# Performance work log

Hardware: AMD Instinct MI355X
Metric: run time of the kernel (lower is better)

The kernel has to match this reference:

```python
import jax, jax.numpy as jnp
import numpy as np

B, T, KD, QD, AD, VD, W = 16, 4096, 1024, 1024, 512, 1024, 8


def moving_sum(x, back, forward):
    # x: [B, T] -> windowed sum over [t-back, t+forward], matches F.conv1d with ones filter
    xp = jnp.pad(x, ((0, 0), (back, forward)))[:, None, :]
    filt = jnp.ones((1, 1, back + forward + 1), x.dtype)
    y = jax.lax.conv_general_dilated(xp, filt, (1,), 'VALID')
    return y[:, 0, :]


def setup_inputs() -> dict:
    key = jax.random.key(0)
    ks = jax.random.split(key, 16)
    inp = {
        'key': jax.random.normal(ks[0], (B, T, KD), jnp.float32),
        'value': jax.random.normal(ks[1], (B, T, VD), jnp.float32),
        'query': jax.random.normal(ks[2], (B, 1, QD), jnp.float32),
        'noise': jax.random.normal(ks[3], (B, T), jnp.float32),
        'Wk_mono': jax.random.normal(ks[4], (KD, AD), jnp.float32) * (KD ** -0.5),
        'b_mono': jnp.zeros((AD,), jnp.float32),
        'Wq_mono': jax.random.normal(ks[5], (QD, AD), jnp.float32) * (QD ** -0.5),
        'Wk_chunk': jax.random.normal(ks[6], (KD, AD), jnp.float32) * (KD ** -0.5),
        'b_chunk': jnp.zeros((AD,), jnp.float32),
        'Wq_chunk': jax.random.normal(ks[7], (QD, AD), jnp.float32) * (QD ** -0.5),
        'r_mono': jnp.array([-4.0], jnp.float32),
        'r_chunk': jnp.array([-4.0], jnp.float32),
    }
    # weight-normalized v vectors: g = sqrt(1/attn_dim), w = g * v/||v||
    g = (1.0 / AD) ** 0.5
    vm = jax.random.normal(ks[8], (AD,), jnp.float32)
    vc = jax.random.normal(ks[9], (AD,), jnp.float32)
    inp['v_mono'] = g * vm / jnp.linalg.norm(vm)
    inp['v_chunk'] = g * vc / jnp.linalg.norm(vc)
    return inp


def _forward(key, value, query, noise, Wk_mono, b_mono, Wq_mono, v_mono, r_mono,
             Wk_chunk, b_chunk, Wq_chunk, v_chunk, r_chunk):
    bs, kmax = key.shape[0], key.shape[1]
    # aw_prev default: one-hot at position 0
    aw_prev = jnp.zeros((bs, kmax), key.dtype).at[:, 0].set(1.0)

    # monotonic energy: [B, T]
    qm = jnp.einsum('bqd,da->bqa', query, Wq_mono)  # [B,1,A], broadcasts over T
    e_mono = jnp.einsum('bta,a->bt', jnp.tanh(key @ Wk_mono + b_mono + qm), v_mono) + r_mono

    # parallel mode: sigmoid with additive gaussian noise
    p_choose = jax.nn.sigmoid(e_mono + noise)
    # safe_cumprod with the original's exclusive_cumsum (prepends ONES, drops last)
    log1mp = jnp.log(jnp.clip(1.0 - p_choose, 1e-10, 1.0))
    shifted = jnp.concatenate([jnp.ones((bs, 1), key.dtype), log1mp[:, :-1]], axis=1)
    cumprod_1mp = jnp.exp(jnp.cumsum(shifted, axis=1))
    aw = p_choose * cumprod_1mp * jnp.cumsum(
        aw_prev / jnp.clip(cumprod_1mp, 1e-10, 1.0), axis=1)

    # chunk energy
    qc = jnp.einsum('bqd,da->bqa', query, Wq_chunk)
    e_chunk = jnp.einsum('bta,a->bt', jnp.tanh(key @ Wk_chunk + b_chunk + qc), v_chunk) + r_chunk

    # efficient chunkwise attention
    u = e_chunk - jnp.max(e_chunk, axis=1, keepdims=True)
    softmax_exp = jnp.maximum(jnp.exp(u), 1e-5)
    denom = moving_sum(softmax_exp, back=W - 1, forward=0)
    beta = softmax_exp * moving_sum(aw / denom, back=0, forward=W - 1)

    cv = jnp.einsum('bt,btd->bd', beta, value)[:, None, :]  # [B,1,VD]
    return cv, aw[..., None]


def reference(key, value, query, noise, Wk_mono, b_mono, Wq_mono, v_mono, r_mono,
              Wk_chunk, b_chunk, Wq_chunk, v_chunk, r_chunk):
    return _forward(key, value, query, noise, Wk_mono, b_mono, Wq_mono, v_mono, r_mono,
                    Wk_chunk, b_chunk, Wq_chunk, v_chunk, r_chunk)
```

## Files before the change

kernel.cpp:

```cpp
#include <hip/hip_runtime.h>
#include <hip/hip_bf16.h>
#include <math.h>

#define B_   16
#define T_   4096
#define KD_  1024
#define AD_  512
#define VD_  1024

typedef float f32x4 __attribute__((ext_vector_type(4)));
typedef short s16x8 __attribute__((ext_vector_type(8)));

static __device__ __forceinline__ short f2bf(float f) {
    __hip_bfloat16 h = __float2bfloat16(f);
    return __builtin_bit_cast(short, h);
}

static __device__ __forceinline__ float fast_tanh(float x) {
    x = fminf(fmaxf(x, -15.f), 15.f);
    float e = __expf(2.f * x);
    return (e - 1.f) / (e + 1.f);
}

static __device__ __forceinline__ void gload16(const void* g, void* l) {
    __builtin_amdgcn_global_load_lds(
        (const __attribute__((address_space(1))) void*)(g),
        (__attribute__((address_space(3))) void*)(l), 16, 0, 0);
}


__global__ __launch_bounds__(256) void cvt_key_blk_kernel(
    const float* __restrict__ key, short* __restrict__ keyB) {
    const size_t nchunk = (size_t)B_ * T_ * KD_ / 8;
    size_t stride = (size_t)gridDim.x * 256;
    for (size_t g = (size_t)blockIdx.x * 256 + threadIdx.x; g < nchunk; g += stride) {
        const float* p = key + g * 8;
        f32x4 f0 = *reinterpret_cast<const f32x4*>(p);
        f32x4 f1 = *reinterpret_cast<const f32x4*>(p + 4);
        s16x8 h;
        h[0] = f2bf(f0[0]); h[1] = f2bf(f0[1]); h[2] = f2bf(f0[2]); h[3] = f2bf(f0[3]);
        h[4] = f2bf(f1[0]); h[5] = f2bf(f1[1]); h[6] = f2bf(f1[2]); h[7] = f2bf(f1[3]);
        size_t m = g >> 7;
        int kc = (int)(g & 127);
        size_t mt = m >> 8;
        int r = (int)(m & 255);
        int kt = kc >> 2;
        int sub = kc & 3;
        int c = (r << 2) | (sub ^ ((r >> 1) & 3));
        *reinterpret_cast<s16x8*>(keyB + (((mt * 32 + kt) * 1024 + c) << 3)) = h;
    }
}

__global__ __launch_bounds__(256) void qproj_kernel(
    const float* __restrict__ query,
    const float* __restrict__ Wq_mono, const float* __restrict__ b_mono,
    const float* __restrict__ Wq_chunk, const float* __restrict__ b_chunk,
    float* __restrict__ qb) {
    __shared__ float red[4][64];
    int b = blockIdx.x;
    int mat = blockIdx.y;
    int ac = blockIdx.z;
    const float* Wq = mat ? Wq_chunk : Wq_mono;
    const float* bb = mat ? b_chunk : b_mono;
    int al = threadIdx.x & 63;
    int dg = threadIdx.x >> 6;
    int a = ac * 64 + al;
    const float* q = query + b * KD_ + dg * 256;
    const float* wp = Wq + (size_t)(dg * 256) * AD_ + a;
    float s = 0.f;
#pragma unroll 4
    for (int d = 0; d < 256; ++d)
        s += q[d] * wp[(size_t)d * AD_];
    red[dg][al] = s;
    __syncthreads();
    if (dg == 0) {
        float t = red[0][al] + red[1][al] + red[2][al] + red[3][al];
        qb[(mat * B_ + b) * AD_ + a] = t + bb[a];
    }
}

__global__ __launch_bounds__(256) void wtrans_kernel(
    const float* __restrict__ Wk_mono, const float* __restrict__ Wk_chunk,
    short* __restrict__ WkTB) {
    __shared__ float tile[32][33];
    int n0 = blockIdx.x * 32;
    int k0 = blockIdx.y * 32;
    int tx = threadIdx.x;
    int ty = threadIdx.y;
    int tid = ty * 32 + tx;
    const float* src;
    int nloc;
    if (n0 < 512) { src = Wk_mono;  nloc = n0; }
    else          { src = Wk_chunk; nloc = n0 - 512; }
#pragma unroll
    for (int i = 0; i < 4; ++i) {
        int k = ty + i * 8;
        tile[k][tx] = src[(size_t)(k0 + k) * AD_ + nloc + tx];
    }
    __syncthreads();
    if (tid < 128) {
        int r = tid >> 2;
        int sub = tid & 3;
        s16x8 h;
#pragma unroll
        for (int j = 0; j < 8; ++j)
            h[j] = f2bf(tile[sub * 8 + j][r]);
        int n = n0 + r;
        int nblk = n >> 8;
        int rloc = n & 255;
        int kt = k0 >> 5;
        int c = (rloc << 2) | (sub ^ ((rloc >> 1) & 3));
        *reinterpret_cast<s16x8*>(WkTB + (((size_t)(nblk * 32 + kt) * 1024 + c) << 3)) = h;
    }
}

__global__ __launch_bounds__(1024, 4) void gemm_e_kernel(
    const short* __restrict__ keyB,
    const short* __restrict__ WkTB,
    const float* __restrict__ qb,
    const float* __restrict__ v_mono, const float* __restrict__ v_chunk,
    float* __restrict__ e_ws ) {
    __shared__ short As[2][1024 * 8];
    __shared__ short Bs[2][1024 * 8];
    int tid = threadIdx.x;
    int bid = blockIdx.x;
    int swz = (bid & 7) * 128 + (bid >> 3);
    int mt = swz >> 2;
    int nt = swz & 3;
    int mBase = mt * 256;
    int nBase = nt * 256;
    int lane = tid & 63;
    int wid = tid >> 6;
    int wr = wid >> 2, wc = wid & 3;
    int col16 = lane & 15, g4 = lane >> 4;

    const short* pA = keyB + ((size_t)mt * 32 * 1024 + tid) * 8;
    const short* pB = WkTB + ((size_t)nt * 32 * 1024 + tid) * 8;
    int sAB = (wid * 64) * 8;

    int aoff[4], boff[4];
#pragma unroll
    for (int m = 0; m < 4; ++m) {
        int row = wr * 64 + m * 16 + col16;
        aoff[m] = (row * 4 + (g4 ^ ((row >> 1) & 3))) * 8;
    }
#pragma unroll
    for (int n = 0; n < 4; ++n) {
        int row = wc * 64 + n * 16 + col16;
        boff[n] = (row * 4 + (g4 ^ ((row >> 1) & 3))) * 8;
    }

    f32x4 zero4 = {0.f, 0.f, 0.f, 0.f};
    f32x4 acc[4][4];
#pragma unroll
    for (int m = 0; m < 4; ++m)
#pragma unroll
        for (int n = 0; n < 4; ++n) acc[m][n] = zero4;

    gload16(pA, &As[0][sAB]);
    gload16(pB, &Bs[0][sAB]);
    pA += 8192; pB += 8192;
    __syncthreads();

    int cur = 0;
    for (int kt = 0; kt < 31; ++kt) {
        int nxt = cur ^ 1;
        gload16(pA, &As[nxt][sAB]);
        gload16(pB, &Bs[nxt][sAB]);
        pA += 8192; pB += 8192;
        s16x8 af[4], bfr[4];
#pragma unroll
        for (int m = 0; m < 4; ++m)
            af[m] = *reinterpret_cast<const s16x8*>(&As[cur][aoff[m]]);
#pragma unroll
        for (int n = 0; n < 4; ++n)
            bfr[n] = *reinterpret_cast<const s16x8*>(&Bs[cur][boff[n]]);
#pragma unroll
        for (int m = 0; m < 4; ++m)
#pragma unroll
            for (int n = 0; n < 4; ++n)
                acc[m][n] = __builtin_amdgcn_mfma_f32_16x16x32_bf16(af[m], bfr[n], acc[m][n], 0, 0, 0);
        __syncthreads();
        cur = nxt;
    }
    {
        s16x8 af[4], bfr[4];
#pragma unroll
        for (int m = 0; m < 4; ++m)
            af[m] = *reinterpret_cast<const s16x8*>(&As[cur][aoff[m]]);
#pragma unroll
        for (int n = 0; n < 4; ++n)
            bfr[n] = *reinterpret_cast<const s16x8*>(&Bs[cur][boff[n]]);
#pragma unroll
        for (int m = 0; m < 4; ++m)
#pragma unroll
            for (int n = 0; n < 4; ++n)
                acc[m][n] = __builtin_amdgcn_mfma_f32_16x16x32_bf16(af[m], bfr[n], acc[m][n], 0, 0, 0);
    }

    int bIdx = mBase >> 12;
    int matrix = nBase >> 9;
    int aBase = (nBase & 511) + wc * 64 + col16;
    const float* qbRow = qb + (matrix * B_ + bIdx) * AD_;
    const float* vv = matrix ? v_chunk : v_mono;
    float* eArr = e_ws + matrix * (B_ * T_);
    float qcol[4], vcol[4];
#pragma unroll
    for (int n = 0; n < 4; ++n) {
        int a = aBase + n * 16;
        qcol[n] = qbRow[a];
        vcol[n] = vv[a];
    }
#pragma unroll
    for (int m = 0; m < 4; ++m) {
        float s0 = 0.f, s1 = 0.f, s2 = 0.f, s3 = 0.f;
#pragma unroll
        for (int n = 0; n < 4; ++n) {
            s0 += fast_tanh(acc[m][n][0] + qcol[n]) * vcol[n];
            s1 += fast_tanh(acc[m][n][1] + qcol[n]) * vcol[n];
            s2 += fast_tanh(acc[m][n][2] + qcol[n]) * vcol[n];
            s3 += fast_tanh(acc[m][n][3] + qcol[n]) * vcol[n];
        }
#pragma unroll
        for (int mask = 1; mask < 16; mask <<= 1) {
            s0 += __shfl_xor(s0, mask, 64);
            s1 += __shfl_xor(s1, mask, 64);
            s2 += __shfl_xor(s2, mask, 64);
            s3 += __shfl_xor(s3, mask, 64);
        }
        if (col16 == 0) {
            int rowB = mBase + wr * 64 + m * 16 + g4 * 4;
            atomicAdd(&eArr[rowB + 0], s0);
            atomicAdd(&eArr[rowB + 1], s1);
            atomicAdd(&eArr[rowB + 2], s2);
            atomicAdd(&eArr[rowB + 3], s3);
        }
    }
}

__global__ __launch_bounds__(256) void scan_kernel(
    const float* __restrict__ e_ws,
    const float* __restrict__ noise,
    const float* __restrict__ r_mono, const float* __restrict__ r_chunk,
    float* __restrict__ aw_out, float* __restrict__ beta_out) {
    __shared__ float s_aw[T_];
    __shared__ float s_sexp[T_];
    __shared__ float s_ad[T_];
    __shared__ float s_w[4];
    int b = blockIdx.x;
    int tid = threadIdx.x;
    int lane = tid & 63;
    int wid4 = tid >> 6;
    int t0 = tid * 16;
    const float* em = e_ws + b * T_;
    const float* ec = e_ws + B_ * T_ + b * T_;
    const float* nz = noise + b * T_;
    float rm = r_mono[0], rc = r_chunk[0];

    float pv[16], lp[16];
    float run = 0.f;
#pragma unroll
    for (int j = 0; j < 16; ++j) {
        float x = em[t0 + j] + rm + nz[t0 + j];
        float p = 1.f / (1.f + expf(-x));
        pv[j] = p;
        float om = fminf(fmaxf(1.f - p, 1e-10f), 1.f);
        lp[j] = run;
        run += logf(om);
    }
    float x = run;
#pragma unroll
    for (int off = 1; off < 64; off <<= 1) {
        float y = __shfl_up(x, off, 64);
        if (lane >= off) x += y;
    }
    if (lane == 63) s_w[wid4] = x;
    __syncthreads();
    float wbase = 0.f;
#pragma unroll
    for (int i = 0; i < 3; ++i) if (i < wid4) wbase += s_w[i];
    float base = 1.f + (wbase + x - run);
#pragma unroll
    for (int j = 0; j < 16; ++j) {
        float aw = pv[j] * expf(base + lp[j]);
        s_aw[t0 + j] = aw;
        aw_out[b * T_ + t0 + j] = aw;
    }
    float evs[16];
    float lmax = -INFINITY;
#pragma unroll
    for (int j = 0; j < 16; ++j) {
        float v = ec[t0 + j] + rc;
        evs[j] = v;
        lmax = fmaxf(lmax, v);
    }
#pragma unroll
    for (int off = 1; off < 64; off <<= 1)
        lmax = fmaxf(lmax, __shfl_xor(lmax, off, 64));
    __syncthreads();
    if (lane == 0) s_w[wid4] = lmax;
    __syncthreads();
    float mx = fmaxf(fmaxf(s_w[0], s_w[1]), fmaxf(s_w[2], s_w[3]));
#pragma unroll
    for (int j = 0; j < 16; ++j)
        s_sexp[t0 + j] = fmaxf(expf(evs[j] - mx), 1e-5f);
    __syncthreads();
#pragma unroll
    for (int j = 0; j < 16; ++j) {
        int t = t0 + j;
        int lo = t - 7; if (lo < 0) lo = 0;
        float d = 0.f;
        for (int i = lo; i <= t; ++i) d += s_sexp[i];
        s_ad[t] = s_aw[t] / d;
    }
    __syncthreads();
#pragma unroll
    for (int j = 0; j < 16; ++j) {
        int t = t0 + j;
        int hi = t + 7; if (hi > T_ - 1) hi = T_ - 1;
        float m2 = 0.f;
        for (int i = t; i <= hi; ++i) m2 += s_ad[i];
        beta_out[b * T_ + t] = s_sexp[t] * m2;
    }
}

__global__ __launch_bounds__(256) void cv_kernel(
    const float* __restrict__ value,
    const float* __restrict__ beta,
    float* __restrict__ cv) {
    __shared__ float s_beta[128];
    int b = blockIdx.x;
    int tc = blockIdx.y;
    int tid = threadIdx.x;
    int t0 = tc * 128;
    if (tid < 128) s_beta[tid] = beta[b * T_ + t0 + tid];
    __syncthreads();
    int d0 = tid * 4;
    f32x4 acc = {0.f, 0.f, 0.f, 0.f};
    const float* vp = value + (size_t)(b * T_ + t0) * VD_ + d0;
#pragma unroll 4
    for (int i = 0; i < 128; ++i) {
        f32x4 v = *reinterpret_cast<const f32x4*>(vp + (size_t)i * VD_);
        float bt = s_beta[i];
        acc[0] += bt * v[0];
        acc[1] += bt * v[1];
        acc[2] += bt * v[2];
        acc[3] += bt * v[3];
    }
    atomicAdd(&cv[b * VD_ + d0 + 0], acc[0]);
    atomicAdd(&cv[b * VD_ + d0 + 1], acc[1]);
    atomicAdd(&cv[b * VD_ + d0 + 2], acc[2]);
    atomicAdd(&cv[b * VD_ + d0 + 3], acc[3]);
}

extern "C" void kernel_launch(void* const* d_in, const int* in_sizes, int n_in,
                              void* d_out, int out_size, void* d_ws, size_t ws_size,
                              hipStream_t stream) {
    const float* key      = (const float*)d_in[0];
    const float* value    = (const float*)d_in[1];
    const float* query    = (const float*)d_in[2];
    const float* noise    = (const float*)d_in[3];
    const float* Wk_mono  = (const float*)d_in[4];
    const float* b_mono   = (const float*)d_in[5];
    const float* Wq_mono  = (const float*)d_in[6];
    const float* Wk_chunk = (const float*)d_in[7];
    const float* b_chunk  = (const float*)d_in[8];
    const float* Wq_chunk = (const float*)d_in[9];
    const float* r_mono   = (const float*)d_in[10];
    const float* r_chunk  = (const float*)d_in[11];
    const float* v_mono   = (const float*)d_in[12];
    const float* v_chunk  = (const float*)d_in[13];
    float* out = (float*)d_out;

    char* ws = (char*)d_ws;
    size_t off = 0;
    float* e_ws = (float*)(ws + off); off += 2 * B_ * T_ * sizeof(float);
    float* qb   = (float*)(ws + off); off += 2 * B_ * AD_ * sizeof(float);
    short* WkTB = (short*)(ws + off); off += (size_t)KD_ * KD_ * 2;
    float* beta = (float*)(ws + off); off += B_ * T_ * sizeof(float);
    short* keyB = (short*)(ws + off);

    hipMemsetAsync(e_ws, 0, 2 * B_ * T_ * sizeof(float), stream);
    hipMemsetAsync(out, 0, B_ * VD_ * sizeof(float), stream);

    qproj_kernel<<<dim3(16, 2, 8), 256, 0, stream>>>(query, Wq_mono, b_mono, Wq_chunk, b_chunk, qb);
    wtrans_kernel<<<dim3(32, 32), dim3(32, 8), 0, stream>>>(Wk_mono, Wk_chunk, WkTB);
    cvt_key_blk_kernel<<<4096, 256, 0, stream>>>(key, keyB);
    gemm_e_kernel<<<1024, 1024, 0, stream>>>(keyB, WkTB, qb, v_mono, v_chunk, e_ws);
    scan_kernel<<<16, 256, 0, stream>>>(e_ws, noise, r_mono, r_chunk, out + B_ * VD_, beta);
    cv_kernel<<<dim3(16, 32), 256, 0, stream>>>(value, beta, out);
}
```

Baseline: 376.9 us.

## Restructure bf16 GEMM into 8-wave ping-pong pipeline with 64-wide K tiles

The key and weight pre-layouts change from 32-wide to 64-wide K tiles with an 8-way XOR swizzle. The energy GEMM moves from 16 waves with 64x64 warp tiles to 8 waves with 128x64 warp tiles. Its main loop becomes a hand-scheduled pipeline: interleaved half-tile global-to-LDS loads, explicit vmcnt waits, sched barriers and raised priority around MFMA clusters. This aims to hide load latency and cut LDS reads and barriers per MFMA. The cost is higher register pressure from 32 accumulators per thread and fragile manual scheduling.

```diff
diff --git a/kernel.cpp b/kernel.cpp
--- a/kernel.cpp
+++ b/kernel.cpp
@@ -44,10 +44,10 @@
         int kc = (int)(g & 127);
         size_t mt = m >> 8;
         int r = (int)(m & 255);
-        int kt = kc >> 2;
-        int sub = kc & 3;
-        int c = (r << 2) | (sub ^ ((r >> 1) & 3));
-        *reinterpret_cast<s16x8*>(keyB + (((mt * 32 + kt) * 1024 + c) << 3)) = h;
+        int ktile = kc >> 3;
+        int sub = kc & 7;
+        int c = (r << 3) | (sub ^ (r & 7));
+        *reinterpret_cast<s16x8*>(keyB + (((mt * 16 + ktile) * 2048 + c) << 3)) = h;
     }
 }
 
@@ -99,29 +99,76 @@
     }
     __syncthreads();
     if (tid < 128) {
-        int r = tid >> 2;
-        int sub = tid & 3;
+        int rl = tid >> 2;
+        int sub2 = tid & 3;
         s16x8 h;
 #pragma unroll
         for (int j = 0; j < 8; ++j)
-            h[j] = f2bf(tile[sub * 8 + j][r]);
-        int n = n0 + r;
-        int nblk = n >> 8;
+            h[j] = f2bf(tile[sub2 * 8 + j][rl]);
+        int n = n0 + rl;
+        int nt = n >> 8;
         int rloc = n & 255;
-        int kt = k0 >> 5;
-        int c = (rloc << 2) | (sub ^ ((rloc >> 1) & 3));
-        *reinterpret_cast<s16x8*>(WkTB + (((size_t)(nblk * 32 + kt) * 1024 + c) << 3)) = h;
-    }
-}
-
-__global__ __launch_bounds__(1024, 4) void gemm_e_kernel(
+        int ktile = k0 >> 6;
+        int sub = ((k0 & 63) >> 3) + sub2;
+        int c = (rloc << 3) | (sub ^ (rloc & 7));
+        *reinterpret_cast<s16x8*>(WkTB + (((size_t)(nt * 16 + ktile) * 2048 + c) << 3)) = h;
+    }
+}
+
+#define SBAR __builtin_amdgcn_sched_barrier(0)
+#define BAR  do { SBAR; __builtin_amdgcn_s_barrier(); SBAR; } while (0)
+#define VM6  asm volatile("s_waitcnt vmcnt(6)" ::: "memory")
+
+#define STAGE_A(buf, kt, h) do { \
+    const short* _g = aT + (((size_t)(kt) * 2048 + (h) * 1024) << 3); \
+    gload16(_g + tid * 8,        &As[buf][(((h) * 1024 + wid * 64)) * 8]); \
+    gload16(_g + (512 + tid) * 8, &As[buf][(((h) * 1024 + 512 + wid * 64)) * 8]); \
+} while (0)
+
+#define STAGE_B(buf, kt, h) do { \
+    const short* _g = bT + (((size_t)(kt) * 2048 + (h) * 1024) << 3); \
+    gload16(_g + tid * 8,        &Bs[buf][(((h) * 1024 + wid * 64)) * 8]); \
+    gload16(_g + (512 + tid) * 8, &Bs[buf][(((h) * 1024 + 512 + wid * 64)) * 8]); \
+} while (0)
+
+#define DS_A(bb, mh) do { \
+    _Pragma("unroll") \
+    for (int _j = 0; _j < 4; ++_j) { \
+        aR[_j][0] = *reinterpret_cast<const s16x8*>(&As[bb][aoff[(mh) * 4 + _j]]); \
+        aR[_j][1] = *reinterpret_cast<const s16x8*>(&As[bb][aoff[(mh) * 4 + _j] ^ 32]); \
+    } \
+} while (0)
+
+#define DS_B(bb, nh) do { \
+    _Pragma("unroll") \
+    for (int _j = 0; _j < 2; ++_j) { \
+        bR[_j][0] = *reinterpret_cast<const s16x8*>(&Bs[bb][boff[(nh) * 2 + _j]]); \
+        bR[_j][1] = *reinterpret_cast<const s16x8*>(&Bs[bb][boff[(nh) * 2 + _j] ^ 32]); \
+    } \
+} while (0)
+
+#define MMA(mh, nh) do { \
+    __builtin_amdgcn_s_setprio(1); \
+    _Pragma("unroll") \
+    for (int _j = 0; _j < 4; ++_j) \
+    _Pragma("unroll") \
+    for (int _n = 0; _n < 2; ++_n) { \
+        acc[(mh) * 4 + _j][(nh) * 2 + _n] = __builtin_amdgcn_mfma_f32_16x16x32_bf16( \
+            aR[_j][0], bR[_n][0], acc[(mh) * 4 + _j][(nh) * 2 + _n], 0, 0, 0); \
+        acc[(mh) * 4 + _j][(nh) * 2 + _n] = __builtin_amdgcn_mfma_f32_16x16x32_bf16( \
+            aR[_j][1], bR[_n][1], acc[(mh) * 4 + _j][(nh) * 2 + _n], 0, 0, 0); \
+    } \
+    __builtin_amdgcn_s_setprio(0); \
+} while (0)
+
+__global__ __launch_bounds__(512) void gemm_e_kernel(
     const short* __restrict__ keyB,
     const short* __restrict__ WkTB,
     const float* __restrict__ qb,
     const float* __restrict__ v_mono, const float* __restrict__ v_chunk,
     float* __restrict__ e_ws ) {
-    __shared__ short As[2][1024 * 8];
-    __shared__ short Bs[2][1024 * 8];
+    __shared__ short As[2][16384];
+    __shared__ short Bs[2][16384];
     int tid = threadIdx.x;
     int bid = blockIdx.x;
     int swz = (bid & 7) * 128 + (bid >> 3);
@@ -134,69 +181,67 @@
     int wr = wid >> 2, wc = wid & 3;
     int col16 = lane & 15, g4 = lane >> 4;
 
-    const short* pA = keyB + ((size_t)mt * 32 * 1024 + tid) * 8;
-    const short* pB = WkTB + ((size_t)nt * 32 * 1024 + tid) * 8;
-    int sAB = (wid * 64) * 8;
-
-    int aoff[4], boff[4];
-#pragma unroll
-    for (int m = 0; m < 4; ++m) {
-        int row = wr * 64 + m * 16 + col16;
-        aoff[m] = (row * 4 + (g4 ^ ((row >> 1) & 3))) * 8;
-    }
-#pragma unroll
-    for (int n = 0; n < 4; ++n) {
-        int row = wc * 64 + n * 16 + col16;
-        boff[n] = (row * 4 + (g4 ^ ((row >> 1) & 3))) * 8;
-    }
-
-    f32x4 zero4 = {0.f, 0.f, 0.f, 0.f};
-    f32x4 acc[4][4];
-#pragma unroll
-    for (int m = 0; m < 4; ++m)
-#pragma unroll
-        for (int n = 0; n < 4; ++n) acc[m][n] = zero4;
-
-    gload16(pA, &As[0][sAB]);
-    gload16(pB, &Bs[0][sAB]);
-    pA += 8192; pB += 8192;
-    __syncthreads();
-
-    int cur = 0;
-    for (int kt = 0; kt < 31; ++kt) {
-        int nxt = cur ^ 1;
-        gload16(pA, &As[nxt][sAB]);
-        gload16(pB, &Bs[nxt][sAB]);
-        pA += 8192; pB += 8192;
-        s16x8 af[4], bfr[4];
-#pragma unroll
-        for (int m = 0; m < 4; ++m)
-            af[m] = *reinterpret_cast<const s16x8*>(&As[cur][aoff[m]]);
-#pragma unroll
-        for (int n = 0; n < 4; ++n)
-            bfr[n] = *reinterpret_cast<const s16x8*>(&Bs[cur][boff[n]]);
-#pragma unroll
-        for (int m = 0; m < 4; ++m)
-#pragma unroll
-            for (int n = 0; n < 4; ++n)
-                acc[m][n] = __builtin_amdgcn_mfma_f32_16x16x32_bf16(af[m], bfr[n], acc[m][n], 0, 0, 0);
-        __syncthreads();
-        cur = nxt;
-    }
-    {
-        s16x8 af[4], bfr[4];
-#pragma unroll
-        for (int m = 0; m < 4; ++m)
-            af[m] = *reinterpret_cast<const s16x8*>(&As[cur][aoff[m]]);
-#pragma unroll
-        for (int n = 0; n < 4; ++n)
-            bfr[n] = *reinterpret_cast<const s16x8*>(&Bs[cur][boff[n]]);
-#pragma unroll
-        for (int m = 0; m < 4; ++m)
-#pragma unroll
-            for (int n = 0; n < 4; ++n)
-                acc[m][n] = __builtin_amdgcn_mfma_f32_16x16x32_bf16(af[m], bfr[n], acc[m][n], 0, 0, 0);
-    }
+    const short* aT = keyB + ((size_t)mt * 16 * 2048 << 3);
+    const short* bT = WkTB + ((size_t)nt * 16 * 2048 << 3);
+
+    int aoff[8], boff[4];
+#pragma unroll
+    for (int fi = 0; fi < 8; ++fi) {
+        int row = wr * 128 + fi * 16 + col16;
+        aoff[fi] = ((row << 3) | (g4 ^ (row & 7))) * 8;
+    }
+#pragma unroll
+    for (int fj = 0; fj < 4; ++fj) {
+        int col = wc * 64 + fj * 16 + col16;
+        boff[fj] = ((col << 3) | (g4 ^ (col & 7))) * 8;
+    }
+
+    f32x4 acc[8][4];
+#pragma unroll
+    for (int i = 0; i < 8; ++i)
+#pragma unroll
+        for (int j = 0; j < 4; ++j) acc[i][j] = (f32x4){0.f, 0.f, 0.f, 0.f};
+
+    s16x8 aR[4][2], bR[2][2];
+
+    STAGE_A(0, 0, 0); STAGE_B(0, 0, 0); STAGE_B(0, 0, 1); STAGE_A(0, 0, 1);
+    STAGE_A(1, 1, 0); STAGE_B(1, 1, 1); STAGE_A(1, 1, 1);
+    VM6;
+    BAR;
+
+    for (int it = 0; it < 8; ++it) {
+        int t1 = 2 * it + 1;
+        int t2 = 2 * it + 2 > 15 ? 15 : 2 * it + 2;
+        int t3 = 2 * it + 3 > 15 ? 15 : 2 * it + 3;
+        DS_A(0, 0); DS_B(0, 0);
+        STAGE_B(1, t1, 0);
+        BAR; MMA(0, 0); BAR;
+        DS_B(0, 1);
+        STAGE_A(0, t2, 0);
+        BAR; MMA(0, 1); BAR;
+        DS_A(0, 1);
+        STAGE_B(0, t2, 1);
+        BAR; MMA(1, 1); BAR;
+        DS_B(0, 0);
+        STAGE_A(0, t2, 1);
+        VM6;
+        BAR; MMA(1, 0); BAR;
+        DS_A(1, 0); DS_B(1, 0);
+        STAGE_B(0, t2, 0);
+        BAR; MMA(0, 0); BAR;
+        DS_B(1, 1);
+        STAGE_A(1, t3, 0);
+        BAR; MMA(0, 1); BAR;
+        DS_A(1, 1);
+        STAGE_B(1, t3, 1);
+        BAR; MMA(1, 1); BAR;
+        DS_B(1, 0);
+        STAGE_A(1, t3, 1);
+        VM6;
+        BAR; MMA(1, 0); BAR;
+    }
+
+    asm volatile("s_waitcnt vmcnt(0)" ::: "memory");
 
     int bIdx = mBase >> 12;
     int matrix = nBase >> 9;
@@ -212,14 +257,14 @@
         vcol[n] = vv[a];
     }
 #pragma unroll
-    for (int m = 0; m < 4; ++m) {
+    for (int fi = 0; fi < 8; ++fi) {
         float s0 = 0.f, s1 = 0.f, s2 = 0.f, s3 = 0.f;
 #pragma unroll
         for (int n = 0; n < 4; ++n) {
-            s0 += fast_tanh(acc[m][n][0] + qcol[n]) * vcol[n];
-            s1 += fast_tanh(acc[m][n][1] + qcol[n]) * vcol[n];
-            s2 += fast_tanh(acc[m][n][2] + qcol[n]) * vcol[n];
-            s3 += fast_tanh(acc[m][n][3] + qcol[n]) * vcol[n];
+            s0 += fast_tanh(acc[fi][n][0] + qcol[n]) * vcol[n];
+            s1 += fast_tanh(acc[fi][n][1] + qcol[n]) * vcol[n];
+            s2 += fast_tanh(acc[fi][n][2] + qcol[n]) * vcol[n];
+            s3 += fast_tanh(acc[fi][n][3] + qcol[n]) * vcol[n];
         }
 #pragma unroll
         for (int mask = 1; mask < 16; mask <<= 1) {
@@ -229,7 +274,7 @@
             s3 += __shfl_xor(s3, mask, 64);
         }
         if (col16 == 0) {
-            int rowB = mBase + wr * 64 + m * 16 + g4 * 4;
+            int rowB = mBase + wr * 128 + fi * 16 + g4 * 4;
             atomicAdd(&eArr[rowB + 0], s0);
             atomicAdd(&eArr[rowB + 1], s1);
             atomicAdd(&eArr[rowB + 2], s2);
@@ -386,7 +431,7 @@
     qproj_kernel<<<dim3(16, 2, 8), 256, 0, stream>>>(query, Wq_mono, b_mono, Wq_chunk, b_chunk, qb);
     wtrans_kernel<<<dim3(32, 32), dim3(32, 8), 0, stream>>>(Wk_mono, Wk_chunk, WkTB);
     cvt_key_blk_kernel<<<4096, 256, 0, stream>>>(key, keyB);
-    gemm_e_kernel<<<1024, 1024, 0, stream>>>(keyB, WkTB, qb, v_mono, v_chunk, e_ws);
+    gemm_e_kernel<<<1024, 512, 0, stream>>>(keyB, WkTB, qb, v_mono, v_chunk, e_ws);
     scan_kernel<<<16, 256, 0, stream>>>(e_ws, noise, r_mono, r_chunk, out + B_ * VD_, beta);
     cv_kernel<<<dim3(16, 32), 256, 0, stream>>>(value, beta, out);
 }
```

Result: faster. 360.9 us (-4.2%).

## Fuse prep kernels and shrink GEMM block to 4 waves with 128x128 warp tiles

Applied to the files above, without the earlier changes.

The key conversion, weight transpose, query projection and two memsets are merged into one prep kernel launch, which removes several launch and memset overheads. The GEMM block goes from 16 waves at 64x64 each to 4 waves at 128x128 each over the same 256x256 tile. This raises register reuse of the LDS fragments per wave but needs 256 accumulator registers per lane, which risks spilling or lower occupancy. Each thread now issues four LDS-direct loads per operand per k-step.

```diff
diff --git a/kernel.cpp b/kernel.cpp
--- a/kernel.cpp
+++ b/kernel.cpp
@@ -29,92 +29,105 @@
 }
 
 
-__global__ __launch_bounds__(256) void cvt_key_blk_kernel(
-    const float* __restrict__ key, short* __restrict__ keyB) {
-    const size_t nchunk = (size_t)B_ * T_ * KD_ / 8;
-    size_t stride = (size_t)gridDim.x * 256;
-    for (size_t g = (size_t)blockIdx.x * 256 + threadIdx.x; g < nchunk; g += stride) {
-        const float* p = key + g * 8;
-        f32x4 f0 = *reinterpret_cast<const f32x4*>(p);
-        f32x4 f1 = *reinterpret_cast<const f32x4*>(p + 4);
-        s16x8 h;
-        h[0] = f2bf(f0[0]); h[1] = f2bf(f0[1]); h[2] = f2bf(f0[2]); h[3] = f2bf(f0[3]);
-        h[4] = f2bf(f1[0]); h[5] = f2bf(f1[1]); h[6] = f2bf(f1[2]); h[7] = f2bf(f1[3]);
-        size_t m = g >> 7;
-        int kc = (int)(g & 127);
-        size_t mt = m >> 8;
-        int r = (int)(m & 255);
-        int kt = kc >> 2;
-        int sub = kc & 3;
-        int c = (r << 2) | (sub ^ ((r >> 1) & 3));
-        *reinterpret_cast<s16x8*>(keyB + (((mt * 32 + kt) * 1024 + c) << 3)) = h;
-    }
-}
-
-__global__ __launch_bounds__(256) void qproj_kernel(
+__global__ __launch_bounds__(256) void prep_kernel(
+    const float* __restrict__ key, short* __restrict__ keyB,
+    const float* __restrict__ Wk_mono, const float* __restrict__ Wk_chunk,
+    short* __restrict__ WkTB,
     const float* __restrict__ query,
     const float* __restrict__ Wq_mono, const float* __restrict__ b_mono,
     const float* __restrict__ Wq_chunk, const float* __restrict__ b_chunk,
-    float* __restrict__ qb) {
-    __shared__ float red[4][64];
-    int b = blockIdx.x;
-    int mat = blockIdx.y;
-    int ac = blockIdx.z;
-    const float* Wq = mat ? Wq_chunk : Wq_mono;
-    const float* bb = mat ? b_chunk : b_mono;
-    int al = threadIdx.x & 63;
-    int dg = threadIdx.x >> 6;
-    int a = ac * 64 + al;
-    const float* q = query + b * KD_ + dg * 256;
-    const float* wp = Wq + (size_t)(dg * 256) * AD_ + a;
-    float s = 0.f;
+    float* __restrict__ qb,
+    float* __restrict__ e_ws, float* __restrict__ outzero) {
+    int bid = blockIdx.x;
+    int tid = threadIdx.x;
+
+    if (bid < 4096) {
+        const size_t nchunk = (size_t)B_ * T_ * KD_ / 8;
+        size_t stride = (size_t)4096 * 256;
+        for (size_t g = (size_t)bid * 256 + tid; g < nchunk; g += stride) {
+            const float* p = key + g * 8;
+            f32x4 f0 = *reinterpret_cast<const f32x4*>(p);
+            f32x4 f1 = *reinterpret_cast<const f32x4*>(p + 4);
+            s16x8 h;
+            h[0] = f2bf(f0[0]); h[1] = f2bf(f0[1]); h[2] = f2bf(f0[2]); h[3] = f2bf(f0[3]);
+            h[4] = f2bf(f1[0]); h[5] = f2bf(f1[1]); h[6] = f2bf(f1[2]); h[7] = f2bf(f1[3]);
+            size_t m = g >> 7;
+            int kc = (int)(g & 127);
+            size_t mt = m >> 8;
+            int r = (int)(m & 255);
+            int kt = kc >> 2;
+            int sub = kc & 3;
+            int c = (r << 2) | (sub ^ ((r >> 1) & 3));
+            *reinterpret_cast<s16x8*>(keyB + (((mt * 32 + kt) * 1024 + c) << 3)) = h;
+        }
+    } else if (bid < 5120) {
+        __shared__ float tile[32][33];
+        int wbid = bid - 4096;
+        int n0 = (wbid & 31) * 32;
+        int k0 = (wbid >> 5) * 32;
+        int tx = tid & 31;
+        int ty = tid >> 5;
+        const float* src;
+        int nloc;
+        if (n0 < 512) { src = Wk_mono;  nloc = n0; }
+        else          { src = Wk_chunk; nloc = n0 - 512; }
+#pragma unroll
+        for (int i = 0; i < 4; ++i) {
+            int k = ty + i * 8;
+            tile[k][tx] = src[(size_t)(k0 + k) * AD_ + nloc + tx];
+        }
+        __syncthreads();
+        if (tid < 128) {
+            int rl = tid >> 2;
+            int sub = tid & 3;
+            s16x8 h;
+#pragma unroll
+            for (int j = 0; j < 8; ++j)
+                h[j] = f2bf(tile[sub * 8 + j][rl]);
+            int n = n0 + rl;
+            int nt = n >> 8;
+            int rloc = n & 255;
+            int kt = k0 >> 5;
+            int c = (rloc << 2) | (sub ^ ((rloc >> 1) & 3));
+            *reinterpret_cast<s16x8*>(WkTB + (((size_t)(nt * 32 + kt) * 1024 + c) << 3)) = h;
+        }
+    } else if (bid < 5376) {
+        __shared__ float red[4][64];
+        int qbid = bid - 5120;
+        int b = qbid & 15;
+        int mat = (qbid >> 4) & 1;
+        int ac = qbid >> 5;
+        const float* Wq = mat ? Wq_chunk : Wq_mono;
+        const float* bb = mat ? b_chunk : b_mono;
+        int al = tid & 63;
+        int dg = tid >> 6;
+        int a = ac * 64 + al;
+        const float* q = query + b * KD_ + dg * 256;
+        const float* wp = Wq + (size_t)(dg * 256) * AD_ + a;
+        float s = 0.f;
 #pragma unroll 4
-    for (int d = 0; d < 256; ++d)
-        s += q[d] * wp[(size_t)d * AD_];
-    red[dg][al] = s;
-    __syncthreads();
-    if (dg == 0) {
-        float t = red[0][al] + red[1][al] + red[2][al] + red[3][al];
-        qb[(mat * B_ + b) * AD_ + a] = t + bb[a];
-    }
-}
-
-__global__ __launch_bounds__(256) void wtrans_kernel(
-    const float* __restrict__ Wk_mono, const float* __restrict__ Wk_chunk,
-    short* __restrict__ WkTB) {
-    __shared__ float tile[32][33];
-    int n0 = blockIdx.x * 32;
-    int k0 = blockIdx.y * 32;
-    int tx = threadIdx.x;
-    int ty = threadIdx.y;
-    int tid = ty * 32 + tx;
-    const float* src;
-    int nloc;
-    if (n0 < 512) { src = Wk_mono;  nloc = n0; }
-    else          { src = Wk_chunk; nloc = n0 - 512; }
-#pragma unroll
-    for (int i = 0; i < 4; ++i) {
-        int k = ty + i * 8;
-        tile[k][tx] = src[(size_t)(k0 + k) * AD_ + nloc + tx];
-    }
-    __syncthreads();
-    if (tid < 128) {
-        int r = tid >> 2;
-        int sub = tid & 3;
-        s16x8 h;
-#pragma unroll
-        for (int j = 0; j < 8; ++j)
-            h[j] = f2bf(tile[sub * 8 + j][r]);
-        int n = n0 + r;
-        int nblk = n >> 8;
-        int rloc = n & 255;
-        int kt = k0 >> 5;
-        int c = (rloc << 2) | (sub ^ ((rloc >> 1) & 3));
-        *reinterpret_cast<s16x8*>(WkTB + (((size_t)(nblk * 32 + kt) * 1024 + c) << 3)) = h;
-    }
-}
-
-__global__ __launch_bounds__(1024, 4) void gemm_e_kernel(
+        for (int d = 0; d < 256; ++d)
+            s += q[d] * wp[(size_t)d * AD_];
+        red[dg][al] = s;
+        __syncthreads();
+        if (dg == 0) {
+            float t = red[0][al] + red[1][al] + red[2][al] + red[3][al];
+            qb[(mat * B_ + b) * AD_ + a] = t + bb[a];
+        }
+    } else {
+        int zbid = bid - 5376;
+        f32x4 z = {0.f, 0.f, 0.f, 0.f};
+        if (zbid < 128) {
+            float* dst = e_ws + (size_t)zbid * 1024 + tid * 4;
+            *reinterpret_cast<f32x4*>(dst) = z;
+        } else {
+            float* dst = outzero + (size_t)(zbid - 128) * 1024 + tid * 4;
+            *reinterpret_cast<f32x4*>(dst) = z;
+        }
+    }
+}
+
+__global__ __launch_bounds__(256) void gemm_e_kernel(
     const short* __restrict__ keyB,
     const short* __restrict__ WkTB,
     const float* __restrict__ qb,
@@ -131,95 +144,104 @@
     int nBase = nt * 256;
     int lane = tid & 63;
     int wid = tid >> 6;
-    int wr = wid >> 2, wc = wid & 3;
+    int wr = wid >> 1, wc = wid & 1;
     int col16 = lane & 15, g4 = lane >> 4;
 
-    const short* pA = keyB + ((size_t)mt * 32 * 1024 + tid) * 8;
-    const short* pB = WkTB + ((size_t)nt * 32 * 1024 + tid) * 8;
-    int sAB = (wid * 64) * 8;
-
-    int aoff[4], boff[4];
-#pragma unroll
-    for (int m = 0; m < 4; ++m) {
-        int row = wr * 64 + m * 16 + col16;
-        aoff[m] = (row * 4 + (g4 ^ ((row >> 1) & 3))) * 8;
-    }
-#pragma unroll
-    for (int n = 0; n < 4; ++n) {
-        int row = wc * 64 + n * 16 + col16;
-        boff[n] = (row * 4 + (g4 ^ ((row >> 1) & 3))) * 8;
-    }
-
-    f32x4 zero4 = {0.f, 0.f, 0.f, 0.f};
-    f32x4 acc[4][4];
-#pragma unroll
-    for (int m = 0; m < 4; ++m)
-#pragma unroll
-        for (int n = 0; n < 4; ++n) acc[m][n] = zero4;
-
-    gload16(pA, &As[0][sAB]);
-    gload16(pB, &Bs[0][sAB]);
-    pA += 8192; pB += 8192;
+    const short* pA[4];
+    const short* pB[4];
+    int sOff[4];
+#pragma unroll
+    for (int i = 0; i < 4; ++i) {
+        pA[i] = keyB + ((size_t)mt * 32 * 1024 + i * 256 + tid) * 8;
+        pB[i] = WkTB + ((size_t)nt * 32 * 1024 + i * 256 + tid) * 8;
+        sOff[i] = (i * 256 + wid * 64) * 8;
+    }
+
+    int aoff[8], boff[8];
+#pragma unroll
+    for (int fi = 0; fi < 8; ++fi) {
+        int row = wr * 128 + fi * 16 + col16;
+        aoff[fi] = (row * 4 + (g4 ^ ((row >> 1) & 3))) * 8;
+    }
+#pragma unroll
+    for (int fj = 0; fj < 8; ++fj) {
+        int coln = wc * 128 + fj * 16 + col16;
+        boff[fj] = (coln * 4 + (g4 ^ ((coln >> 1) & 3))) * 8;
+    }
+
+    f32x4 acc[8][8];
+#pragma unroll
+    for (int i = 0; i < 8; ++i)
+#pragma unroll
+        for (int j = 0; j < 8; ++j) acc[i][j] = (f32x4){0.f, 0.f, 0.f, 0.f};
+
+#pragma unroll
+    for (int i = 0; i < 4; ++i) {
+        gload16(pA[i], &As[0][sOff[i]]);
+        gload16(pB[i], &Bs[0][sOff[i]]);
+        pA[i] += 8192; pB[i] += 8192;
+    }
     __syncthreads();
 
     int cur = 0;
     for (int kt = 0; kt < 31; ++kt) {
         int nxt = cur ^ 1;
-        gload16(pA, &As[nxt][sAB]);
-        gload16(pB, &Bs[nxt][sAB]);
-        pA += 8192; pB += 8192;
-        s16x8 af[4], bfr[4];
-#pragma unroll
-        for (int m = 0; m < 4; ++m)
-            af[m] = *reinterpret_cast<const s16x8*>(&As[cur][aoff[m]]);
-#pragma unroll
-        for (int n = 0; n < 4; ++n)
-            bfr[n] = *reinterpret_cast<const s16x8*>(&Bs[cur][boff[n]]);
-#pragma unroll
-        for (int m = 0; m < 4; ++m)
-#pragma unroll
-            for (int n = 0; n < 4; ++n)
-                acc[m][n] = __builtin_amdgcn_mfma_f32_16x16x32_bf16(af[m], bfr[n], acc[m][n], 0, 0, 0);
+#pragma unroll
+        for (int i = 0; i < 4; ++i) {
+            gload16(pA[i], &As[nxt][sOff[i]]);
+            gload16(pB[i], &Bs[nxt][sOff[i]]);
+            pA[i] += 8192; pB[i] += 8192;
+        }
+        s16x8 bfr[8];
+#pragma unroll
+        for (int fj = 0; fj < 8; ++fj)
+            bfr[fj] = *reinterpret_cast<const s16x8*>(&Bs[cur][boff[fj]]);
+#pragma unroll
+        for (int fi = 0; fi < 8; ++fi) {
+            s16x8 af = *reinterpret_cast<const s16x8*>(&As[cur][aoff[fi]]);
+#pragma unroll
+            for (int fj = 0; fj < 8; ++fj)
+                acc[fi][fj] = __builtin_amdgcn_mfma_f32_16x16x32_bf16(af, bfr[fj], acc[fi][fj], 0, 0, 0);
+        }
         __syncthreads();
         cur = nxt;
     }
     {
-        s16x8 af[4], bfr[4];
-#pragma unroll
-        for (int m = 0; m < 4; ++m)
-            af[m] = *reinterpret_cast<const s16x8*>(&As[cur][aoff[m]]);
-#pragma unroll
-        for (int n = 0; n < 4; ++n)
-            bfr[n] = *reinterpret_cast<const s16x8*>(&Bs[cur][boff[n]]);
-#pragma unroll
-        for (int m = 0; m < 4; ++m)
-#pragma unroll
-            for (int n = 0; n < 4; ++n)
-                acc[m][n] = __builtin_amdgcn_mfma_f32_16x16x32_bf16(af[m], bfr[n], acc[m][n], 0, 0, 0);
+        s16x8 bfr[8];
+#pragma unroll
+        for (int fj = 0; fj < 8; ++fj)
+            bfr[fj] = *reinterpret_cast<const s16x8*>(&Bs[cur][boff[fj]]);
+#pragma unroll
+        for (int fi = 0; fi < 8; ++fi) {
+            s16x8 af = *reinterpret_cast<const s16x8*>(&As[cur][aoff[fi]]);
+#pragma unroll
+            for (int fj = 0; fj < 8; ++fj)
+                acc[fi][fj] = __builtin_amdgcn_mfma_f32_16x16x32_bf16(af, bfr[fj], acc[fi][fj], 0, 0, 0);
+        }
     }
 
     int bIdx = mBase >> 12;
     int matrix = nBase >> 9;
-    int aBase = (nBase & 511) + wc * 64 + col16;
+    int aBase = (nBase & 511) + wc * 128 + col16;
     const float* qbRow = qb + (matrix * B_ + bIdx) * AD_;
     const float* vv = matrix ? v_chunk : v_mono;
     float* eArr = e_ws + matrix * (B_ * T_);
-    float qcol[4], vcol[4];
-#pragma unroll
-    for (int n = 0; n < 4; ++n) {
-        int a = aBase + n * 16;
-        qcol[n] = qbRow[a];
-        vcol[n] = vv[a];
-    }
-#pragma unroll
-    for (int m = 0; m < 4; ++m) {
+    float qcol[8], vcol[8];
+#pragma unroll
+    for (int fj = 0; fj < 8; ++fj) {
+        int a = aBase + fj * 16;
+        qcol[fj] = qbRow[a];
+        vcol[fj] = vv[a];
+    }
+#pragma unroll
+    for (int fi = 0; fi < 8; ++fi) {
         float s0 = 0.f, s1 = 0.f, s2 = 0.f, s3 = 0.f;
 #pragma unroll
-        for (int n = 0; n < 4; ++n) {
-            s0 += fast_tanh(acc[m][n][0] + qcol[n]) * vcol[n];
-            s1 += fast_tanh(acc[m][n][1] + qcol[n]) * vcol[n];
-            s2 += fast_tanh(acc[m][n][2] + qcol[n]) * vcol[n];
-            s3 += fast_tanh(acc[m][n][3] + qcol[n]) * vcol[n];
+        for (int fj = 0; fj < 8; ++fj) {
+            s0 += fast_tanh(acc[fi][fj][0] + qcol[fj]) * vcol[fj];
+            s1 += fast_tanh(acc[fi][fj][1] + qcol[fj]) * vcol[fj];
+            s2 += fast_tanh(acc[fi][fj][2] + qcol[fj]) * vcol[fj];
+            s3 += fast_tanh(acc[fi][fj][3] + qcol[fj]) * vcol[fj];
         }
 #pragma unroll
         for (int mask = 1; mask < 16; mask <<= 1) {
@@ -229,7 +251,7 @@
             s3 += __shfl_xor(s3, mask, 64);
         }
         if (col16 == 0) {
-            int rowB = mBase + wr * 64 + m * 16 + g4 * 4;
+            int rowB = mBase + wr * 128 + fi * 16 + g4 * 4;
             atomicAdd(&eArr[rowB + 0], s0);
             atomicAdd(&eArr[rowB + 1], s1);
             atomicAdd(&eArr[rowB + 2], s2);
@@ -380,13 +402,10 @@
     float* beta = (float*)(ws + off); off += B_ * T_ * sizeof(float);
     short* keyB = (short*)(ws + off);
 
-    hipMemsetAsync(e_ws, 0, 2 * B_ * T_ * sizeof(float), stream);
-    hipMemsetAsync(out, 0, B_ * VD_ * sizeof(float), stream);
-
-    qproj_kernel<<<dim3(16, 2, 8), 256, 0, stream>>>(query, Wq_mono, b_mono, Wq_chunk, b_chunk, qb);
-    wtrans_kernel<<<dim3(32, 32), dim3(32, 8), 0, stream>>>(Wk_mono, Wk_chunk, WkTB);
-    cvt_key_blk_kernel<<<4096, 256, 0, stream>>>(key, keyB);
-    gemm_e_kernel<<<1024, 1024, 0, stream>>>(keyB, WkTB, qb, v_mono, v_chunk, e_ws);
+    prep_kernel<<<5520, 256, 0, stream>>>(key, keyB, Wk_mono, Wk_chunk, WkTB,
+                                          query, Wq_mono, b_mono, Wq_chunk, b_chunk, qb,
+                                          e_ws, out);
+    gemm_e_kernel<<<1024, 256, 0, stream>>>(keyB, WkTB, qb, v_mono, v_chunk, e_ws);
     scan_kernel<<<16, 256, 0, stream>>>(e_ws, noise, r_mono, r_chunk, out + B_ * VD_, beta);
     cv_kernel<<<dim3(16, 32), 256, 0, stream>>>(value, beta, out);
 }
```

After: 406.1 us. 1.08x slower.
